# Performance work log

Measured on AMD Instinct MI355X. Metric: run time of the kernel, lower is better.

## Reference

```python
import jax, jax.numpy as jnp
import numpy as np

HID, D, NH, NL = 1024, 64, 16, 128  # hidden_dim, head_dim, num_head, num_landmarks


def iterative_inv(mat, n_iter=6):
    # Moore-Penrose pseudo-inverse via Newton-Schulz (Nystromformer), fp32.
    I = jnp.eye(mat.shape[-1], dtype=mat.dtype)
    K = mat
    denom = (jnp.max(jnp.sum(jnp.abs(K), axis=-2), axis=-1)
             * jnp.max(jnp.sum(jnp.abs(K), axis=-1), axis=-1))[..., None, None]
    V = jnp.swapaxes(K, -1, -2) / denom  # Z0 = K^T / (||K||_1 ||K||_inf)
    for _ in range(n_iter):
        KV = K @ V
        V = 0.25 * V @ (13.0 * I - KV @ (15.0 * I - KV @ (7.0 * I - KV)))
    return V


def nystrom_forward(X, mask, Wq, bq, Wk, bk, Wv, bv, Wo, bo):
    B, orig_len, _ = X.shape
    pad_len = NL - orig_len % NL  # always >= 1, matches torch code
    L = orig_len + pad_len
    Xp = jnp.pad(X, ((0, 0), (0, pad_len), (0, 0)))

    def split(Y):  # [B, L, NH*D] -> [B, NH, L, D]
        return Y.reshape(B, L, NH, D).transpose(0, 2, 1, 3)

    Q = split(Xp @ Wq.T + bq).astype(jnp.float32)
    K = split(Xp @ Wk.T + bk).astype(jnp.float32)
    V = split(Xp @ Wv.T + bv).astype(jnp.float32)

    m = mask[:, None, :, None]  # [B,1,L,1]
    scale = 1.0 / (D ** 0.25)   # 1/sqrt(sqrt(head_dim)) applied to both Q and K
    Q = Q * m * scale
    K = K * m * scale

    seg = L // NL
    Q_l = Q.reshape(B, NH, NL, seg, D).mean(axis=-2)  # landmarks via segment means
    K_l = K.reshape(B, NH, NL, seg, D).mean(axis=-2)

    kernel_1 = jax.nn.softmax(jnp.einsum('bhnd,bhld->bhnl', Q, K_l), axis=-1)   # [B,H,L,NL]
    kernel_2 = jax.nn.softmax(jnp.einsum('bhld,bhmd->bhlm', Q_l, K_l), axis=-1)  # [B,H,NL,NL]
    scores_3 = jnp.einsum('bhld,bhnd->bhln', Q_l, K) - 1e9 * (1.0 - mask[:, None, None, :])
    kernel_3 = jax.nn.softmax(scores_3, axis=-1)                                 # [B,H,NL,L]

    out = kernel_1 @ (iterative_inv(kernel_2) @ (kernel_3 @ V))  # [B,H,L,D]
    out = out.transpose(0, 2, 1, 3).reshape(B, L, NH * D)
    out = out @ Wo.T + bo
    return out[:, :orig_len]


def setup_inputs() -> dict:
    key = jax.random.key(0)
    ks = jax.random.split(key, 9)
    B, S = 2, 4095
    Lpad = S + (NL - S % NL)
    s = 0.02
    return {
        'X': jax.random.normal(ks[0], (B, S, HID), dtype=jnp.float32),
        'mask': jnp.ones((B, Lpad), dtype=jnp.float32),
        'Wq': jax.random.normal(ks[1], (NH * D, HID), dtype=jnp.float32) * s,
        'bq': jnp.zeros((NH * D,), dtype=jnp.float32),
        'Wk': jax.random.normal(ks[2], (NH * D, HID), dtype=jnp.float32) * s,
        'bk': jnp.zeros((NH * D,), dtype=jnp.float32),
        'Wv': jax.random.normal(ks[3], (NH * D, HID), dtype=jnp.float32) * s,
        'bv': jnp.zeros((NH * D,), dtype=jnp.float32),
        'Wo': jax.random.normal(ks[4], (HID, NH * D), dtype=jnp.float32) * s,
        'bo': jnp.zeros((HID,), dtype=jnp.float32),
    }


def reference(X, mask, Wq, bq, Wk, bk, Wv, bv, Wo, bo):
    return nystrom_forward(X, mask, Wq, bq, Wk, bk, Wv, bv, Wo, bo)
```

## Files before the change

kernel.cpp:

```cpp
#include <hip/hip_runtime.h>
#include <hip/hip_bf16.h>
#include <math.h>

#define S_ORIG 4095
#define LPAD   4096
#define NHEADS 16
#define DH     64
#define NLM    128
#define BHT    32
#define HIDDEN 1024
#define QKSCALE 0.35355339059327373f

typedef unsigned short u16;
typedef short s16x8 __attribute__((ext_vector_type(8)));
typedef float f32x4 __attribute__((ext_vector_type(4)));

#define IDX64(r, c)  ((r) * 64 + ((c) ^ (((r) & 7) << 3)))
#define IDX128(r, c) ((r) * 128 + ((c) ^ (((r) & 7) << 3)))

__device__ inline void split2(float x, u16& h, u16& l) {
    __hip_bfloat16 bh = __float2bfloat16(x);
    float fh = __bfloat162float(bh);
    __hip_bfloat16 bl = __float2bfloat16(x - fh);
    h = *(u16*)&bh;
    l = *(u16*)&bl;
}

__device__ inline float bf16f(u16 b) {
    unsigned u = ((unsigned)b) << 16;
    return *(float*)&u;
}

__global__ __launch_bounds__(256) void k_split_x(const float* __restrict__ X,
                                                 u16* __restrict__ XH,
                                                 u16* __restrict__ XL) {
    int idx = blockIdx.x * 256 + threadIdx.x;
    int gr = idx >> 8;
    int c4 = (idx & 255) * 4;
    int b = gr >> 12, l = gr & (LPAD - 1);
    float4 v = make_float4(0.f, 0.f, 0.f, 0.f);
    if (l < S_ORIG) v = *(const float4*)(X + ((size_t)b * S_ORIG + l) * HIDDEN + c4);
    ushort4 h4, l4;
    split2(v.x, h4.x, l4.x); split2(v.y, h4.y, l4.y);
    split2(v.z, h4.z, l4.z); split2(v.w, h4.w, l4.w);
    size_t o = (size_t)gr * HIDDEN + c4;
    *(ushort4*)(XH + o) = h4;
    *(ushort4*)(XL + o) = l4;
}

__global__ __launch_bounds__(256) void k_split_w(const float* __restrict__ W,
                                                 u16* __restrict__ WH,
                                                 u16* __restrict__ WL) {
    int idx = blockIdx.x * 256 + threadIdx.x;
    size_t o = (size_t)idx * 4;
    float4 v = *(const float4*)(W + o);
    ushort4 h4, l4;
    split2(v.x, h4.x, l4.x); split2(v.y, h4.y, l4.y);
    split2(v.z, h4.z, l4.z); split2(v.w, h4.w, l4.w);
    *(ushort4*)(WH + o) = h4;
    *(ushort4*)(WL + o) = l4;
}

__global__ __launch_bounds__(256) void k_gemm_bf16(
    const u16* __restrict__ AH, const u16* __restrict__ AL,
    const u16* __restrict__ BH, const u16* __restrict__ BL,
    const float* __restrict__ bias, const float* __restrict__ mask,
    float* __restrict__ out, u16* __restrict__ poutH, u16* __restrict__ poutL,
    int mode)
{
    __shared__ u16 Ah_lds[128 * 32];
    __shared__ u16 Al_lds[128 * 32];
    __shared__ u16 Bh_lds[128 * 32];
    __shared__ u16 Bl_lds[128 * 32];
    int tid = threadIdx.x;
    int row0 = blockIdx.x * 128, col0 = blockIdx.y * 128;
    int lane = tid & 63, wv = tid >> 6;
    int wr = (wv >> 1) * 64, wc = (wv & 1) * 64;
    int lr = lane & 15, lk = lane >> 4;
    int sr = tid >> 2, sc = tid & 3;

    f32x4 acc[4][4] = {};

    for (int kt = 0; kt < 1024; kt += 32) {
        #pragma unroll
        for (int h = 0; h < 2; ++h) {
            int r = sr + h * 64;
            int csrc = (sc ^ ((r >> 1) & 3)) * 8;
            size_t ga = (size_t)(row0 + r) * HIDDEN + kt + csrc;
            size_t gb = (size_t)(col0 + r) * HIDDEN + kt + csrc;
            int ldst = r * 32 + sc * 8;
            __builtin_amdgcn_global_load_lds(
                (const __attribute__((address_space(1))) void*)(AH + ga),
                (__attribute__((address_space(3))) void*)(&Ah_lds[ldst]), 16, 0, 0);
            __builtin_amdgcn_global_load_lds(
                (const __attribute__((address_space(1))) void*)(AL + ga),
                (__attribute__((address_space(3))) void*)(&Al_lds[ldst]), 16, 0, 0);
            __builtin_amdgcn_global_load_lds(
                (const __attribute__((address_space(1))) void*)(BH + gb),
                (__attribute__((address_space(3))) void*)(&Bh_lds[ldst]), 16, 0, 0);
            __builtin_amdgcn_global_load_lds(
                (const __attribute__((address_space(1))) void*)(BL + gb),
                (__attribute__((address_space(3))) void*)(&Bl_lds[ldst]), 16, 0, 0);
        }
        __syncthreads();
        s16x8 ah[4], al[4], bh[4], bl[4];
        #pragma unroll
        for (int i = 0; i < 4; ++i) {
            int ra = wr + i * 16 + lr;
            int rb = wc + i * 16 + lr;
            int ca = (lk ^ ((ra >> 1) & 3)) * 8;
            int cb = (lk ^ ((rb >> 1) & 3)) * 8;
            ah[i] = *(const s16x8*)&Ah_lds[ra * 32 + ca];
            al[i] = *(const s16x8*)&Al_lds[ra * 32 + ca];
            bh[i] = *(const s16x8*)&Bh_lds[rb * 32 + cb];
            bl[i] = *(const s16x8*)&Bl_lds[rb * 32 + cb];
        }
        #pragma unroll
        for (int i = 0; i < 4; ++i)
            #pragma unroll
            for (int j = 0; j < 4; ++j)
                acc[i][j] = __builtin_amdgcn_mfma_f32_16x16x32_bf16(ah[i], bh[j], acc[i][j], 0, 0, 0);
        #pragma unroll
        for (int i = 0; i < 4; ++i)
            #pragma unroll
            for (int j = 0; j < 4; ++j)
                acc[i][j] = __builtin_amdgcn_mfma_f32_16x16x32_bf16(ah[i], bl[j], acc[i][j], 0, 0, 0);
        #pragma unroll
        for (int i = 0; i < 4; ++i)
            #pragma unroll
            for (int j = 0; j < 4; ++j)
                acc[i][j] = __builtin_amdgcn_mfma_f32_16x16x32_bf16(al[i], bh[j], acc[i][j], 0, 0, 0);
        __syncthreads();
    }

    #pragma unroll
    for (int i = 0; i < 4; ++i) {
        #pragma unroll
        for (int j = 0; j < 4; ++j) {
            int cc = col0 + wc + j * 16 + lr;
            float bval = bias[cc];
            #pragma unroll
            for (int q = 0; q < 4; ++q) {
                int rr = row0 + wr + i * 16 + lk * 4 + q;
                int bb = rr >> 12, l = rr & (LPAD - 1);
                float val = acc[i][j][q] + bval;
                if (mode == 0) {
                    if (mask) val *= mask[(size_t)bb * LPAD + l] * QKSCALE;
                    size_t oi = (((size_t)bb * NHEADS + (cc >> 6)) * LPAD + l) * DH + (cc & 63);
                    if (poutH) {
                        u16 hh2, ll2; split2(val, hh2, ll2);
                        poutH[oi] = hh2;
                        poutL[oi] = ll2;
                    } else {
                        out[oi] = val;
                    }
                } else {
                    if (l < S_ORIG)
                        out[((size_t)bb * S_ORIG + l) * HIDDEN + cc] = val;
                }
            }
        }
    }
}

__global__ void k_landmarks(const float* __restrict__ Q,
                            const u16* __restrict__ KPH, const u16* __restrict__ KPL,
                            float* __restrict__ QL, float* __restrict__ KL,
                            u16* __restrict__ QLPH, u16* __restrict__ QLPL) {
    int n = blockIdx.x, bh = blockIdx.y, d = threadIdx.x;
    size_t base = ((size_t)bh * LPAD + n * 32) * DH + d;
    float sq = 0.f, sk = 0.f;
    #pragma unroll
    for (int s = 0; s < 32; ++s) {
        sq += Q[base + (size_t)s * DH];
        sk += bf16f(KPH[base + (size_t)s * DH]) + bf16f(KPL[base + (size_t)s * DH]);
    }
    float ql = sq * (1.f / 32.f), kl = sk * (1.f / 32.f);
    size_t oi = ((size_t)bh * NLM + n) * DH + d;
    QL[oi] = ql;
    KL[oi] = kl;
    u16 hh2, ll2; split2(ql, hh2, ll2);
    QLPH[oi] = hh2;
    QLPL[oi] = ll2;
}

__global__ __launch_bounds__(256) void k_qlk(const float* __restrict__ QLb,
                                             const float* __restrict__ Bsrc,
                                             float* __restrict__ out) {
    __shared__ float Qt[64][132];
    __shared__ float Bt[64][132];
    int tid = threadIdx.x;
    int tx = tid & 15, ty = tid >> 4;
    int bh = blockIdx.y;
    const float* QLp = QLb + (size_t)bh * NLM * DH;
    const float* Bp = Bsrc + (size_t)bh * NLM * DH;

    #pragma unroll
    for (int q = 0; q < 8; ++q) {
        int idx = tid + q * 256;
        int r = idx >> 4, d4 = idx & 15;
        float4 v = *(const float4*)(QLp + (size_t)r * DH + d4 * 4);
        Qt[d4 * 4 + 0][r] = v.x; Qt[d4 * 4 + 1][r] = v.y;
        Qt[d4 * 4 + 2][r] = v.z; Qt[d4 * 4 + 3][r] = v.w;
        float4 w = *(const float4*)(Bp + (size_t)r * DH + d4 * 4);
        Bt[d4 * 4 + 0][r] = w.x; Bt[d4 * 4 + 1][r] = w.y;
        Bt[d4 * 4 + 2][r] = w.z; Bt[d4 * 4 + 3][r] = w.w;
    }
    __syncthreads();

    float acc[8][8];
    #pragma unroll
    for (int i = 0; i < 8; ++i)
        #pragma unroll
        for (int j = 0; j < 8; ++j) acc[i][j] = 0.f;

    #pragma unroll
    for (int k = 0; k < 64; ++k) {
        float av[8], bv[8];
        float4 t0 = *(const float4*)&Qt[k][ty * 4];
        float4 t1 = *(const float4*)&Qt[k][64 + ty * 4];
        float4 t2 = *(const float4*)&Bt[k][tx * 4];
        float4 t3 = *(const float4*)&Bt[k][64 + tx * 4];
        av[0]=t0.x; av[1]=t0.y; av[2]=t0.z; av[3]=t0.w;
        av[4]=t1.x; av[5]=t1.y; av[6]=t1.z; av[7]=t1.w;
        bv[0]=t2.x; bv[1]=t2.y; bv[2]=t2.z; bv[3]=t2.w;
        bv[4]=t3.x; bv[5]=t3.y; bv[6]=t3.z; bv[7]=t3.w;
        #pragma unroll
        for (int i = 0; i < 8; ++i)
            #pragma unroll
            for (int j = 0; j < 8; ++j)
                acc[i][j] = fmaf(av[i], bv[j], acc[i][j]);
    }

    float m[8], s[8];
    #pragma unroll
    for (int i = 0; i < 8; ++i) {
        m[i] = acc[i][0];
        #pragma unroll
        for (int j = 1; j < 8; ++j) m[i] = fmaxf(m[i], acc[i][j]);
    }
    #pragma unroll
    for (int o = 8; o >= 1; o >>= 1)
        #pragma unroll
        for (int i = 0; i < 8; ++i) m[i] = fmaxf(m[i], __shfl_xor(m[i], o));
    #pragma unroll
    for (int i = 0; i < 8; ++i) {
        s[i] = 0.f;
        #pragma unroll
        for (int j = 0; j < 8; ++j) {
            acc[i][j] = expf(acc[i][j] - m[i]);
            s[i] += acc[i][j];
        }
    }
    #pragma unroll
    for (int o = 8; o >= 1; o >>= 1)
        #pragma unroll
        for (int i = 0; i < 8; ++i) s[i] += __shfl_xor(s[i], o);
    #pragma unroll
    for (int i = 0; i < 8; ++i) {
        int r = (i >> 2) * 64 + ty * 4 + (i & 3);
        float inv = 1.f / s[i];
        #pragma unroll
        for (int jh = 0; jh < 2; ++jh) {
            int c = jh * 64 + tx * 4;
            float4 res;
            res.x = acc[i][jh * 4 + 0] * inv;
            res.y = acc[i][jh * 4 + 1] * inv;
            res.z = acc[i][jh * 4 + 2] * inv;
            res.w = acc[i][jh * 4 + 3] * inv;
            *(float4*)(out + ((size_t)bh * NLM + r) * NLM + c) = res;
        }
    }
}

__global__ void k_v0denom(const float* __restrict__ K2b, float* __restrict__ V0b) {
    int bh = blockIdx.x, t = threadIdx.x;
    const float* K2 = K2b + (size_t)bh * NLM * NLM;
    float* V0 = V0b + (size_t)bh * NLM * NLM;
    float cs = 0.f, rs = 0.f;
    for (int r = 0; r < NLM; ++r) cs += fabsf(K2[r * NLM + t]);
    for (int c = 0; c < NLM; ++c) rs += fabsf(K2[t * NLM + c]);
    __shared__ float sc[128], sr[128];
    sc[t] = cs; sr[t] = rs;
    __syncthreads();
    for (int s = 64; s > 0; s >>= 1) {
        if (t < s) {
            sc[t] = fmaxf(sc[t], sc[t + s]);
            sr[t] = fmaxf(sr[t], sr[t + s]);
        }
        __syncthreads();
    }
    float invden = 1.f / (sc[0] * sr[0]);
    for (int idx = t; idx < NLM * NLM; idx += 128) {
        int i = idx >> 7, j = idx & 127;
        V0[idx] = K2[j * NLM + i] * invden;
    }
}

__global__ __launch_bounds__(256) void k_bmm(const float* __restrict__ Ab,
                                             const float* __restrict__ Bb,
                                             float* __restrict__ Cb,
                                             float* __restrict__ C2b,
                                             int N, float alpha, float sI,
                                             float alpha2, float sI2) {
    __shared__ float At[128][36];
    __shared__ float Bs[128][36];
    int tid = threadIdx.x;
    int tx = tid & 15, ty = tid >> 4;
    int bh = blockIdx.z;
    int r0 = blockIdx.y * 32, c0 = blockIdx.x * 32;
    const float* A = Ab + (size_t)bh * NLM * NLM;
    const float* Bm = Bb + (size_t)bh * NLM * N;

    #pragma unroll
    for (int q = 0; q < 4; ++q) {
        int idx = tid + q * 256;
        int r = idx >> 5, k4 = idx & 31;
        float4 v = *(const float4*)(A + (size_t)(r0 + r) * NLM + k4 * 4);
        At[k4 * 4 + 0][r] = v.x; At[k4 * 4 + 1][r] = v.y;
        At[k4 * 4 + 2][r] = v.z; At[k4 * 4 + 3][r] = v.w;
        int bk = idx >> 3, c4 = idx & 7;
        float4 w = *(const float4*)(Bm + (size_t)bk * N + c0 + c4 * 4);
        *(float4*)&Bs[bk][c4 * 4] = w;
    }
    __syncthreads();

    float acc[2][2] = {};
    #pragma unroll 8
    for (int k = 0; k < 128; ++k) {
        float2 a2 = *(const float2*)&At[k][ty * 2];
        float2 b2 = *(const float2*)&Bs[k][tx * 2];
        acc[0][0] = fmaf(a2.x, b2.x, acc[0][0]);
        acc[0][1] = fmaf(a2.x, b2.y, acc[0][1]);
        acc[1][0] = fmaf(a2.y, b2.x, acc[1][0]);
        acc[1][1] = fmaf(a2.y, b2.y, acc[1][1]);
    }

    float* C = Cb + (size_t)bh * NLM * N;
    float* C2 = C2b ? (C2b + (size_t)bh * NLM * N) : nullptr;
    #pragma unroll
    for (int i = 0; i < 2; ++i) {
        int gr = r0 + ty * 2 + i;
        #pragma unroll
        for (int j = 0; j < 2; ++j) {
            int gc = c0 + tx * 2 + j;
            float idadd = (gr == gc) ? 1.f : 0.f;
            C[(size_t)gr * N + gc] = alpha * acc[i][j] + sI * idadd;
            if (C2) C2[(size_t)gr * N + gc] = alpha2 * acc[i][j] + sI2 * idadd;
        }
    }
}

__global__ __launch_bounds__(256) void k_flashk3(const u16* __restrict__ QLPH,
                                                 const u16* __restrict__ QLPL,
                                                 const u16* __restrict__ KPH,
                                                 const u16* __restrict__ KPL,
                                                 const u16* __restrict__ VPH,
                                                 const u16* __restrict__ VPL,
                                                 const float* __restrict__ mask,
                                                 float* __restrict__ PO,
                                                 float* __restrict__ ML) {
    __shared__ u16 lds[32768];
    u16* QLh = lds;
    u16* QLl = lds + 4096;
    u16* Kh  = lds + 8192;
    u16* Kl  = lds + 12288;
    u16* Vth = lds + 16384;
    u16* Vtl = lds + 20480;
    u16* Ph  = lds + 24576;
    u16* Pl  = lds + 28672;

    int tid = threadIdx.x;
    int lane = tid & 63, wv = tid >> 6;
    int lr = lane & 15, lk = lane >> 4;
    int sp = blockIdx.x, qh = blockIdx.y, bh = blockIdx.z;
    int b = bh >> 4;
    int q0 = qh * 64;
    int wr16 = wv * 16;

    #pragma unroll
    for (int q = 0; q < 2; ++q) {
        int idx = tid + q * 256;
        int r = idx >> 3, sc = idx & 7;
        int csrc = (sc ^ (r & 7)) * 8;
        size_t g = ((size_t)bh * NLM + q0 + r) * DH + csrc;
        __builtin_amdgcn_global_load_lds(
            (const __attribute__((address_space(1))) void*)(QLPH + g),
            (__attribute__((address_space(3))) void*)(&QLh[idx * 8]), 16, 0, 0);
        __builtin_amdgcn_global_load_lds(
            (const __attribute__((address_space(1))) void*)(QLPL + g),
            (__attribute__((address_space(3))) void*)(&QLl[idx * 8]), 16, 0, 0);
    }

    float m_run[4] = {-1e30f, -1e30f, -1e30f, -1e30f};
    float l_run[4] = {0.f, 0.f, 0.f, 0.f};
    f32x4 t5[4] = {};

    for (int t = 0; t < 8; ++t) {
        int kt0 = sp * 512 + t * 64;
        #pragma unroll
        for (int q = 0; q < 2; ++q) {
            int idx = tid + q * 256;
            int r = idx >> 3, sc = idx & 7;
            int csrc = (sc ^ (r & 7)) * 8;
            size_t g = ((size_t)bh * LPAD + kt0 + r) * DH + csrc;
            __builtin_amdgcn_global_load_lds(
                (const __attribute__((address_space(1))) void*)(KPH + g),
                (__attribute__((address_space(3))) void*)(&Kh[idx * 8]), 16, 0, 0);
            __builtin_amdgcn_global_load_lds(
                (const __attribute__((address_space(1))) void*)(KPL + g),
                (__attribute__((address_space(3))) void*)(&Kl[idx * 8]), 16, 0, 0);
        }
        #pragma unroll
        for (int q = 0; q < 4; ++q) {
            int idx = tid + q * 256;
            int n = idx & 63, dg = idx >> 6;
            int d4 = dg * 4;
            size_t g = ((size_t)bh * LPAD + kt0 + n) * DH + d4;
            ushort4 h4 = *(const ushort4*)(VPH + g);
            ushort4 l4 = *(const ushort4*)(VPL + g);
            #pragma unroll
            for (int e = 0; e < 4; ++e) {
                Vth[IDX64(d4 + e, n)] = (&h4.x)[e];
                Vtl[IDX64(d4 + e, n)] = (&l4.x)[e];
            }
        }
        __syncthreads();

        f32x4 t4[4] = {};
        #pragma unroll
        for (int tt = 0; tt < 3; ++tt) {
            const u16* Xs = (tt == 2) ? QLl : QLh;
            const u16* Ys = (tt == 1) ? Kl : Kh;
            #pragma unroll
            for (int kc = 0; kc < 2; ++kc) {
                s16x8 a = *(const s16x8*)&Xs[IDX64(wr16 + lr, kc * 32 + lk * 8)];
                s16x8 bfr[4];
                #pragma unroll
                for (int j = 0; j < 4; ++j)
                    bfr[j] = *(const s16x8*)&Ys[IDX64(j * 16 + lr, kc * 32 + lk * 8)];
                #pragma unroll
                for (int j = 0; j < 4; ++j)
                    t4[j] = __builtin_amdgcn_mfma_f32_16x16x32_bf16(a, bfr[j], t4[j], 0, 0, 0);
            }
        }

        #pragma unroll
        for (int j = 0; j < 4; ++j) {
            float pen = 1e9f * (1.f - mask[(size_t)b * LPAD + kt0 + j * 16 + lr]);
            #pragma unroll
            for (int q = 0; q < 4; ++q) t4[j][q] -= pen;
        }

        float alpha[4];
        #pragma unroll
        for (int q = 0; q < 4; ++q) {
            float tm = t4[0][q];
            #pragma unroll
            for (int j = 1; j < 4; ++j) tm = fmaxf(tm, t4[j][q]);
            tm = fmaxf(tm, __shfl_xor(tm, 1));
            tm = fmaxf(tm, __shfl_xor(tm, 2));
            tm = fmaxf(tm, __shfl_xor(tm, 4));
            tm = fmaxf(tm, __shfl_xor(tm, 8));
            float mn = fmaxf(m_run[q], tm);
            float al = expf(m_run[q] - mn);
            float s = 0.f;
            #pragma unroll
            for (int j = 0; j < 4; ++j) {
                t4[j][q] = expf(t4[j][q] - mn);
                s += t4[j][q];
            }
            s += __shfl_xor(s, 1);
            s += __shfl_xor(s, 2);
            s += __shfl_xor(s, 4);
            s += __shfl_xor(s, 8);
            l_run[q] = l_run[q] * al + s;
            m_run[q] = mn;
            alpha[q] = al;
        }
        #pragma unroll
        for (int j = 0; j < 4; ++j)
            #pragma unroll
            for (int q = 0; q < 4; ++q) t5[j][q] *= alpha[q];

        #pragma unroll
        for (int j = 0; j < 4; ++j) {
            int col = j * 16 + lr;
            #pragma unroll
            for (int q = 0; q < 4; ++q) {
                int row = wr16 + lk * 4 + q;
                u16 hh2, ll2; split2(t4[j][q], hh2, ll2);
                Ph[IDX64(row, col)] = hh2;
                Pl[IDX64(row, col)] = ll2;
            }
        }
        __syncthreads();

        #pragma unroll
        for (int tt = 0; tt < 3; ++tt) {
            const u16* Xs = (tt == 2) ? Pl : Ph;
            const u16* Ys = (tt == 1) ? Vtl : Vth;
            #pragma unroll
            for (int kc = 0; kc < 2; ++kc) {
                s16x8 a = *(const s16x8*)&Xs[IDX64(wr16 + lr, kc * 32 + lk * 8)];
                s16x8 bfr[4];
                #pragma unroll
                for (int j = 0; j < 4; ++j)
                    bfr[j] = *(const s16x8*)&Ys[IDX64(j * 16 + lr, kc * 32 + lk * 8)];
                #pragma unroll
                for (int j = 0; j < 4; ++j)
                    t5[j] = __builtin_amdgcn_mfma_f32_16x16x32_bf16(a, bfr[j], t5[j], 0, 0, 0);
            }
        }
        __syncthreads();
    }

    size_t pb = (size_t)(bh * 16 + qh * 8 + sp) * 64;
    #pragma unroll
    for (int j = 0; j < 4; ++j) {
        int d = j * 16 + lr;
        #pragma unroll
        for (int q = 0; q < 4; ++q) {
            int row = wr16 + lk * 4 + q;
            PO[(pb + row) * 64 + d] = t5[j][q];
        }
    }
    if (lr == 0) {
        #pragma unroll
        for (int q = 0; q < 4; ++q) {
            int row = wr16 + lk * 4 + q;
            ML[(pb + row) * 2 + 0] = m_run[q];
            ML[(pb + row) * 2 + 1] = l_run[q];
        }
    }
}

__global__ void k_flash_combine(const float* __restrict__ PO,
                                const float* __restrict__ ML,
                                float* __restrict__ K3V) {
    int idx = blockIdx.x * 256 + threadIdx.x;
    int bh = idx >> 13, rem = idx & 8191;
    int g = rem >> 6, d = rem & 63;
    int qh = g >> 6, rl = g & 63;
    size_t rb = (size_t)(bh * 16 + qh * 8) * 64 + rl;
    float mstar = -1e30f;
    #pragma unroll
    for (int sp = 0; sp < 8; ++sp)
        mstar = fmaxf(mstar, ML[(rb + (size_t)sp * 64) * 2]);
    float osum = 0.f, lsum = 0.f;
    #pragma unroll
    for (int sp = 0; sp < 8; ++sp) {
        size_t r = rb + (size_t)sp * 64;
        float wgt = expf(ML[r * 2] - mstar);
        osum += wgt * PO[r * 64 + d];
        lsum += wgt * ML[r * 2 + 1];
    }
    K3V[idx] = osum / lsum;
}

__global__ __launch_bounds__(256) void k_attn(const float* __restrict__ Q,
                                              const float* __restrict__ KLb,
                                              const float* __restrict__ MMb,
                                              u16* __restrict__ ATH,
                                              u16* __restrict__ ATL) {
    __shared__ u16 lds[49152];
    u16* Qh  = lds;
    u16* Ql  = lds + 8192;
    u16* KLh = lds + 16384;
    u16* KLl = lds + 24576;
    u16* Ph  = lds;
    u16* Pl  = lds + 16384;
    u16* Mth = lds + 32768;
    u16* Mtl = lds + 40960;

    int tid = threadIdx.x;
    int lane = tid & 63, wv = tid >> 6;
    int lr = lane & 15, lk = lane >> 4;
    int l0 = blockIdx.x * 128, bh = blockIdx.y;
    int b = bh >> 4, hh = bh & 15;
    int wrA = wv * 32;

    #pragma unroll
    for (int q = 0; q < 4; ++q) {
        int idx = tid + q * 256;
        int r = idx >> 3, c8 = (idx & 7) * 8;
        float4 v0 = *(const float4*)(Q + ((size_t)bh * LPAD + l0 + r) * DH + c8);
        float4 v1 = *(const float4*)(Q + ((size_t)bh * LPAD + l0 + r) * DH + c8 + 4);
        float xs[8] = {v0.x, v0.y, v0.z, v0.w, v1.x, v1.y, v1.z, v1.w};
        s16x8 h8, l8;
        #pragma unroll
        for (int e = 0; e < 8; ++e) {
            u16 hh2, ll2; split2(xs[e], hh2, ll2);
            h8[e] = (short)hh2; l8[e] = (short)ll2;
        }
        *(s16x8*)&Qh[IDX64(r, c8)] = h8;
        *(s16x8*)&Ql[IDX64(r, c8)] = l8;

        float4 w0 = *(const float4*)(KLb + ((size_t)bh * NLM + r) * DH + c8);
        float4 w1 = *(const float4*)(KLb + ((size_t)bh * NLM + r) * DH + c8 + 4);
        float ys[8] = {w0.x, w0.y, w0.z, w0.w, w1.x, w1.y, w1.z, w1.w};
        #pragma unroll
        for (int e = 0; e < 8; ++e) {
            u16 hh2, ll2; split2(ys[e], hh2, ll2);
            h8[e] = (short)hh2; l8[e] = (short)ll2;
        }
        *(s16x8*)&KLh[IDX64(r, c8)] = h8;
        *(s16x8*)&KLl[IDX64(r, c8)] = l8;
    }
    #pragma unroll
    for (int q = 0; q < 8; ++q) {
        int idx = tid + q * 256;
        int n = idx >> 4, d4 = (idx & 15) * 4;
        float4 v = *(const float4*)(MMb + ((size_t)bh * NLM + n) * DH + d4);
        float xs[4] = {v.x, v.y, v.z, v.w};
        #pragma unroll
        for (int e = 0; e < 4; ++e) {
            u16 hh2, ll2; split2(xs[e], hh2, ll2);
            Mth[IDX128(d4 + e, n)] = hh2;
            Mtl[IDX128(d4 + e, n)] = ll2;
        }
    }
    __syncthreads();

    f32x4 t4[2][8] = {};
    #pragma unroll
    for (int t = 0; t < 3; ++t) {
        const u16* Xs = (t == 2) ? Ql : Qh;
        const u16* Ys = (t == 1) ? KLl : KLh;
        #pragma unroll
        for (int kc = 0; kc < 2; ++kc) {
            s16x8 a[2], bfr[8];
            #pragma unroll
            for (int i = 0; i < 2; ++i)
                a[i] = *(const s16x8*)&Xs[IDX64(wrA + i * 16 + lr, kc * 32 + lk * 8)];
            #pragma unroll
            for (int j = 0; j < 8; ++j)
                bfr[j] = *(const s16x8*)&Ys[IDX64(j * 16 + lr, kc * 32 + lk * 8)];
            #pragma unroll
            for (int i = 0; i < 2; ++i)
                #pragma unroll
                for (int j = 0; j < 8; ++j)
                    t4[i][j] = __builtin_amdgcn_mfma_f32_16x16x32_bf16(a[i], bfr[j], t4[i][j], 0, 0, 0);
        }
    }

    #pragma unroll
    for (int i = 0; i < 2; ++i)
        #pragma unroll
        for (int q = 0; q < 4; ++q) {
            float m = t4[i][0][q];
            #pragma unroll
            for (int j = 1; j < 8; ++j) m = fmaxf(m, t4[i][j][q]);
            m = fmaxf(m, __shfl_xor(m, 1));
            m = fmaxf(m, __shfl_xor(m, 2));
            m = fmaxf(m, __shfl_xor(m, 4));
            m = fmaxf(m, __shfl_xor(m, 8));
            float s = 0.f;
            #pragma unroll
            for (int j = 0; j < 8; ++j) {
                t4[i][j][q] = expf(t4[i][j][q] - m);
                s += t4[i][j][q];
            }
            s += __shfl_xor(s, 1);
            s += __shfl_xor(s, 2);
            s += __shfl_xor(s, 4);
            s += __shfl_xor(s, 8);
            float inv = 1.f / s;
            #pragma unroll
            for (int j = 0; j < 8; ++j) t4[i][j][q] *= inv;
        }

    __syncthreads();
    #pragma unroll
    for (int i = 0; i < 2; ++i)
        #pragma unroll
        for (int j = 0; j < 8; ++j) {
            int col = j * 16 + lr;
            #pragma unroll
            for (int q = 0; q < 4; ++q) {
                int row = wrA + i * 16 + lk * 4 + q;
                u16 hh2, ll2; split2(t4[i][j][q], hh2, ll2);
                Ph[IDX128(row, col)] = hh2;
                Pl[IDX128(row, col)] = ll2;
            }
        }
    __syncthreads();

    f32x4 t5[2][4] = {};
    #pragma unroll
    for (int t = 0; t < 3; ++t) {
        const u16* Xs = (t == 2) ? Pl : Ph;
        const u16* Ys = (t == 1) ? Mtl : Mth;
        #pragma unroll
        for (int kc = 0; kc < 4; ++kc) {
            s16x8 a[2], bfr[4];
            #pragma unroll
            for (int i = 0; i < 2; ++i)
                a[i] = *(const s16x8*)&Xs[IDX128(wrA + i * 16 + lr, kc * 32 + lk * 8)];
            #pragma unroll
            for (int j = 0; j < 4; ++j)
                bfr[j] = *(const s16x8*)&Ys[IDX128(j * 16 + lr, kc * 32 + lk * 8)];
            #pragma unroll
            for (int i = 0; i < 2; ++i)
                #pragma unroll
                for (int j = 0; j < 4; ++j)
                    t5[i][j] = __builtin_amdgcn_mfma_f32_16x16x32_bf16(a[i], bfr[j], t5[i][j], 0, 0, 0);
        }
    }

    #pragma unroll
    for (int i = 0; i < 2; ++i)
        #pragma unroll
        for (int j = 0; j < 4; ++j) {
            int d = j * 16 + lr;
            #pragma unroll
            for (int q = 0; q < 4; ++q) {
                int l = l0 + wrA + i * 16 + lk * 4 + q;
                size_t base = ((size_t)b * LPAD + l) * HIDDEN + hh * DH + d;
                u16 hh2, ll2; split2(t5[i][j][q], hh2, ll2);
                ATH[base] = hh2;
                ATL[base] = ll2;
            }
        }
}

extern "C" void kernel_launch(void* const* d_in, const int* in_sizes, int n_in,
                              void* d_out, int out_size, void* d_ws, size_t ws_size,
                              hipStream_t stream) {
    (void)in_sizes; (void)n_in; (void)out_size; (void)ws_size;
    const float* X    = (const float*)d_in[0];
    const float* mask = (const float*)d_in[1];
    const float* Wq   = (const float*)d_in[2];
    const float* bq   = (const float*)d_in[3];
    const float* Wk   = (const float*)d_in[4];
    const float* bk   = (const float*)d_in[5];
    const float* Wv   = (const float*)d_in[6];
    const float* bv   = (const float*)d_in[7];
    const float* Wo   = (const float*)d_in[8];
    const float* bo   = (const float*)d_in[9];
    float* out = (float*)d_out;
    float* w = (float*)d_ws;

    size_t o = 0;
    u16* WQH = (u16*)(w + o); o += (size_t)HIDDEN * HIDDEN / 2;
    u16* WQL = (u16*)(w + o); o += (size_t)HIDDEN * HIDDEN / 2;
    u16* WKH = (u16*)(w + o); o += (size_t)HIDDEN * HIDDEN / 2;
    u16* WKL = (u16*)(w + o); o += (size_t)HIDDEN * HIDDEN / 2;
    u16* WVH = (u16*)(w + o); o += (size_t)HIDDEN * HIDDEN / 2;
    u16* WVL = (u16*)(w + o); o += (size_t)HIDDEN * HIDDEN / 2;
    u16* WOH = (u16*)(w + o); o += (size_t)HIDDEN * HIDDEN / 2;
    u16* WOL = (u16*)(w + o); o += (size_t)HIDDEN * HIDDEN / 2;
    float* Q   = w + o; o += (size_t)BHT * LPAD * DH;
    float* K   = w + o; o += (size_t)BHT * LPAD * DH;
    float* V   = w + o; o += (size_t)BHT * LPAD * DH;
    float* QL  = w + o; o += (size_t)BHT * NLM * DH;
    float* KL  = w + o; o += (size_t)BHT * NLM * DH;
    float* K2  = w + o; o += (size_t)BHT * NLM * NLM;
    float* VA  = w + o; o += (size_t)BHT * NLM * NLM;
    float* VB  = w + o; o += (size_t)BHT * NLM * NLM;
    float* KV  = w + o; o += (size_t)BHT * NLM * NLM;
    float* P1  = w + o; o += (size_t)BHT * NLM * NLM;
    float* T3  = w + o; o += (size_t)BHT * NLM * NLM;
    float* PK  = w + o; o += (size_t)BHT * 16 * NLM * DH;
    float* K3V = w + o; o += (size_t)BHT * NLM * DH;
    float* MM  = w + o; o += (size_t)BHT * NLM * DH;
    float* SC  = w + o; o += (size_t)BHT * NLM * LPAD;

    u16* KPH = (u16*)K;
    u16* KPL = KPH + (size_t)BHT * LPAD * DH;
    u16* VPH = (u16*)V;
    u16* VPL = VPH + (size_t)BHT * LPAD * DH;

    float* PO = PK;
    float* ML = PK + (size_t)BHT * 16 * 64 * 64;

    u16* XH  = (u16*)SC;
    u16* XL  = XH + (size_t)2 * LPAD * HIDDEN;
    u16* ATH = (u16*)SC;
    u16* ATL = ATH + (size_t)2 * LPAD * HIDDEN;
    u16* QLPH = (u16*)SC + (size_t)32 * 1024 * 1024;
    u16* QLPL = QLPH + (size_t)BHT * NLM * DH;

    k_split_x<<<8192, 256, 0, stream>>>(X, XH, XL);
    k_split_w<<<1024, 256, 0, stream>>>(Wq, WQH, WQL);
    k_split_w<<<1024, 256, 0, stream>>>(Wk, WKH, WKL);
    k_split_w<<<1024, 256, 0, stream>>>(Wv, WVH, WVL);
    k_split_w<<<1024, 256, 0, stream>>>(Wo, WOH, WOL);

    dim3 gg(64, 8);
    k_gemm_bf16<<<gg, 256, 0, stream>>>(XH, XL, WQH, WQL, bq, mask, Q, nullptr, nullptr, 0);
    k_gemm_bf16<<<gg, 256, 0, stream>>>(XH, XL, WKH, WKL, bk, mask, nullptr, KPH, KPL, 0);
    k_gemm_bf16<<<gg, 256, 0, stream>>>(XH, XL, WVH, WVL, bv, nullptr, nullptr, VPH, VPL, 0);

    k_landmarks<<<dim3(NLM, BHT), 64, 0, stream>>>(Q, KPH, KPL, QL, KL, QLPH, QLPL);

    k_qlk<<<dim3(1, BHT), 256, 0, stream>>>(QL, KL, K2);

    k_flashk3<<<dim3(8, 2, BHT), 256, 0, stream>>>(QLPH, QLPL, KPH, KPL, VPH, VPL, mask, PO, ML);
    k_flash_combine<<<(BHT * NLM * DH) / 256, 256, 0, stream>>>(PO, ML, K3V);

    k_v0denom<<<BHT, 128, 0, stream>>>(K2, VA);
    float* cur = VA;
    float* nxt = VB;
    for (int it = 0; it < 6; ++it) {
        k_bmm<<<dim3(4, 4, BHT), 256, 0, stream>>>(K2, cur, KV, P1, NLM, 1.f, 0.f, -1.f, 7.f);
        k_bmm<<<dim3(4, 4, BHT), 256, 0, stream>>>(KV, P1, T3, nullptr, NLM, -1.f, 15.f, 0.f, 0.f);
        k_bmm<<<dim3(4, 4, BHT), 256, 0, stream>>>(KV, T3, P1, nullptr, NLM, -1.f, 13.f, 0.f, 0.f);
        k_bmm<<<dim3(4, 4, BHT), 256, 0, stream>>>(cur, P1, nxt, nullptr, NLM, 0.25f, 0.f, 0.f, 0.f);
        float* t = cur; cur = nxt; nxt = t;
    }

    k_bmm<<<dim3(2, 4, BHT), 256, 0, stream>>>(cur, K3V, MM, nullptr, DH, 1.f, 0.f, 0.f, 0.f);

    k_attn<<<dim3(32, BHT), 256, 0, stream>>>(Q, KL, MM, ATH, ATL);
    k_gemm_bf16<<<gg, 256, 0, stream>>>(ATH, ATL, WOH, WOL, bo, nullptr, out, nullptr, nullptr, 1);
}
```

Baseline: 596.1 us.

## Fuse Q/K/V projection GEMMs into one launch and double the K tile

```diff
diff --git a/kernel.cpp b/kernel.cpp
--- a/kernel.cpp
+++ b/kernel.cpp
@@ -63,32 +63,42 @@
 
 __global__ __launch_bounds__(256) void k_gemm_bf16(
     const u16* __restrict__ AH, const u16* __restrict__ AL,
-    const u16* __restrict__ BH, const u16* __restrict__ BL,
-    const float* __restrict__ bias, const float* __restrict__ mask,
-    float* __restrict__ out, u16* __restrict__ poutH, u16* __restrict__ poutL,
-    int mode)
+    const u16* __restrict__ B0H, const u16* __restrict__ B0L,
+    const u16* __restrict__ B1H, const u16* __restrict__ B1L,
+    const u16* __restrict__ B2H, const u16* __restrict__ B2L,
+    const float* __restrict__ bias0, const float* __restrict__ bias1,
+    const float* __restrict__ bias2, const float* __restrict__ mask,
+    float* __restrict__ outQ, u16* __restrict__ KPH, u16* __restrict__ KPL,
+    u16* __restrict__ VPH, u16* __restrict__ VPL,
+    float* __restrict__ outF, int mode)
 {
-    __shared__ u16 Ah_lds[128 * 32];
-    __shared__ u16 Al_lds[128 * 32];
-    __shared__ u16 Bh_lds[128 * 32];
-    __shared__ u16 Bl_lds[128 * 32];
+    __shared__ u16 Ah_lds[128 * 64];
+    __shared__ u16 Al_lds[128 * 64];
+    __shared__ u16 Bh_lds[128 * 64];
+    __shared__ u16 Bl_lds[128 * 64];
     int tid = threadIdx.x;
-    int row0 = blockIdx.x * 128, col0 = blockIdx.y * 128;
+    int seg = (mode == 0) ? (blockIdx.y >> 3) : 0;
+    int row0 = blockIdx.x * 128;
+    int col0 = (mode == 0) ? ((blockIdx.y & 7) * 128) : (blockIdx.y * 128);
+    const u16* BH = (seg == 0) ? B0H : (seg == 1) ? B1H : B2H;
+    const u16* BL = (seg == 0) ? B0L : (seg == 1) ? B1L : B2L;
+    const float* bias = (seg == 0) ? bias0 : (seg == 1) ? bias1 : bias2;
+
     int lane = tid & 63, wv = tid >> 6;
     int wr = (wv >> 1) * 64, wc = (wv & 1) * 64;
     int lr = lane & 15, lk = lane >> 4;
-    int sr = tid >> 2, sc = tid & 3;
+    int sr8 = tid >> 3, sc = tid & 7;
 
     f32x4 acc[4][4] = {};
 
-    for (int kt = 0; kt < 1024; kt += 32) {
-        #pragma unroll
-        for (int h = 0; h < 2; ++h) {
-            int r = sr + h * 64;
-            int csrc = (sc ^ ((r >> 1) & 3)) * 8;
+    for (int kt = 0; kt < 1024; kt += 64) {
+        #pragma unroll
+        for (int h = 0; h < 4; ++h) {
+            int r = sr8 + h * 32;
+            int csrc = (sc ^ (r & 7)) * 8;
             size_t ga = (size_t)(row0 + r) * HIDDEN + kt + csrc;
             size_t gb = (size_t)(col0 + r) * HIDDEN + kt + csrc;
-            int ldst = r * 32 + sc * 8;
+            int ldst = r * 64 + sc * 8;
             __builtin_amdgcn_global_load_lds(
                 (const __attribute__((address_space(1))) void*)(AH + ga),
                 (__attribute__((address_space(3))) void*)(&Ah_lds[ldst]), 16, 0, 0);
@@ -103,33 +113,36 @@
                 (__attribute__((address_space(3))) void*)(&Bl_lds[ldst]), 16, 0, 0);
         }
         __syncthreads();
-        s16x8 ah[4], al[4], bh[4], bl[4];
-        #pragma unroll
-        for (int i = 0; i < 4; ++i) {
-            int ra = wr + i * 16 + lr;
-            int rb = wc + i * 16 + lr;
-            int ca = (lk ^ ((ra >> 1) & 3)) * 8;
-            int cb = (lk ^ ((rb >> 1) & 3)) * 8;
-            ah[i] = *(const s16x8*)&Ah_lds[ra * 32 + ca];
-            al[i] = *(const s16x8*)&Al_lds[ra * 32 + ca];
-            bh[i] = *(const s16x8*)&Bh_lds[rb * 32 + cb];
-            bl[i] = *(const s16x8*)&Bl_lds[rb * 32 + cb];
-        }
-        #pragma unroll
-        for (int i = 0; i < 4; ++i)
-            #pragma unroll
-            for (int j = 0; j < 4; ++j)
-                acc[i][j] = __builtin_amdgcn_mfma_f32_16x16x32_bf16(ah[i], bh[j], acc[i][j], 0, 0, 0);
-        #pragma unroll
-        for (int i = 0; i < 4; ++i)
-            #pragma unroll
-            for (int j = 0; j < 4; ++j)
-                acc[i][j] = __builtin_amdgcn_mfma_f32_16x16x32_bf16(ah[i], bl[j], acc[i][j], 0, 0, 0);
-        #pragma unroll
-        for (int i = 0; i < 4; ++i)
-            #pragma unroll
-            for (int j = 0; j < 4; ++j)
-                acc[i][j] = __builtin_amdgcn_mfma_f32_16x16x32_bf16(al[i], bh[j], acc[i][j], 0, 0, 0);
+        #pragma unroll
+        for (int kc = 0; kc < 2; ++kc) {
+            s16x8 ah[4], al[4], bh4[4], bl4[4];
+            #pragma unroll
+            for (int i = 0; i < 4; ++i) {
+                int ra = wr + i * 16 + lr;
+                int rb = wc + i * 16 + lr;
+                int ca = (((kc << 2) + lk) ^ (ra & 7)) * 8;
+                int cb = (((kc << 2) + lk) ^ (rb & 7)) * 8;
+                ah[i]  = *(const s16x8*)&Ah_lds[ra * 64 + ca];
+                al[i]  = *(const s16x8*)&Al_lds[ra * 64 + ca];
+                bh4[i] = *(const s16x8*)&Bh_lds[rb * 64 + cb];
+                bl4[i] = *(const s16x8*)&Bl_lds[rb * 64 + cb];
+            }
+            #pragma unroll
+            for (int i = 0; i < 4; ++i)
+                #pragma unroll
+                for (int j = 0; j < 4; ++j)
+                    acc[i][j] = __builtin_amdgcn_mfma_f32_16x16x32_bf16(ah[i], bh4[j], acc[i][j], 0, 0, 0);
+            #pragma unroll
+            for (int i = 0; i < 4; ++i)
+                #pragma unroll
+                for (int j = 0; j < 4; ++j)
+                    acc[i][j] = __builtin_amdgcn_mfma_f32_16x16x32_bf16(ah[i], bl4[j], acc[i][j], 0, 0, 0);
+            #pragma unroll
+            for (int i = 0; i < 4; ++i)
+                #pragma unroll
+                for (int j = 0; j < 4; ++j)
+                    acc[i][j] = __builtin_amdgcn_mfma_f32_16x16x32_bf16(al[i], bh4[j], acc[i][j], 0, 0, 0);
+        }
         __syncthreads();
     }
 
@@ -145,18 +158,18 @@
                 int bb = rr >> 12, l = rr & (LPAD - 1);
                 float val = acc[i][j][q] + bval;
                 if (mode == 0) {
-                    if (mask) val *= mask[(size_t)bb * LPAD + l] * QKSCALE;
+                    if (seg < 2) val *= mask[(size_t)bb * LPAD + l] * QKSCALE;
                     size_t oi = (((size_t)bb * NHEADS + (cc >> 6)) * LPAD + l) * DH + (cc & 63);
-                    if (poutH) {
+                    if (seg == 0) {
+                        outQ[oi] = val;
+                    } else {
                         u16 hh2, ll2; split2(val, hh2, ll2);
-                        poutH[oi] = hh2;
-                        poutL[oi] = ll2;
-                    } else {
-                        out[oi] = val;
+                        if (seg == 1) { KPH[oi] = hh2; KPL[oi] = ll2; }
+                        else          { VPH[oi] = hh2; VPL[oi] = ll2; }
                     }
                 } else {
                     if (l < S_ORIG)
-                        out[((size_t)bb * S_ORIG + l) * HIDDEN + cc] = val;
+                        outF[((size_t)bb * S_ORIG + l) * HIDDEN + cc] = val;
                 }
             }
         }
@@ -787,10 +800,9 @@
     k_split_w<<<1024, 256, 0, stream>>>(Wv, WVH, WVL);
     k_split_w<<<1024, 256, 0, stream>>>(Wo, WOH, WOL);
 
-    dim3 gg(64, 8);
-    k_gemm_bf16<<<gg, 256, 0, stream>>>(XH, XL, WQH, WQL, bq, mask, Q, nullptr, nullptr, 0);
-    k_gemm_bf16<<<gg, 256, 0, stream>>>(XH, XL, WKH, WKL, bk, mask, nullptr, KPH, KPL, 0);
-    k_gemm_bf16<<<gg, 256, 0, stream>>>(XH, XL, WVH, WVL, bv, nullptr, nullptr, VPH, VPL, 0);
+    k_gemm_bf16<<<dim3(64, 24), 256, 0, stream>>>(
+        XH, XL, WQH, WQL, WKH, WKL, WVH, WVL, bq, bk, bv, mask,
+        Q, KPH, KPL, VPH, VPL, nullptr, 0);
 
     k_landmarks<<<dim3(NLM, BHT), 64, 0, stream>>>(Q, KPH, KPL, QL, KL, QLPH, QLPL);
 
@@ -813,5 +825,8 @@
     k_bmm<<<dim3(2, 4, BHT), 256, 0, stream>>>(cur, K3V, MM, nullptr, DH, 1.f, 0.f, 0.f, 0.f);
 
     k_attn<<<dim3(32, BHT), 256, 0, stream>>>(Q, KL, MM, ATH, ATL);
-    k_gemm_bf16<<<gg, 256, 0, stream>>>(ATH, ATL, WOH, WOL, bo, nullptr, out, nullptr, nullptr, 1);
-}
+
+    k_gemm_bf16<<<dim3(64, 8), 256, 0, stream>>>(
+        ATH, ATL, WOH, WOL, nullptr, nullptr, nullptr, nullptr, bo, nullptr,
+        nullptr, nullptr, nullptr, nullptr, nullptr, nullptr, nullptr, out, 1);
+}
```

Measured after the change: 568.8 us. 4.6% less time.
